# Performance work log

Measured on AMD Instinct MI355X. Metric: run time of the kernel, lower is better.

The kernel has to match this reference:

```python
import jax, jax.numpy as jnp
import numpy as np

N = 50000        # nodes
E = 800000       # edges
IN_C = 128       # in_channels
HID = 256        # hidden_channels
HEADS = 4
HD = HID // HEADS
LAYERS = 4
GRAPHS = 64
OUT_C = 32
MAX_POS = 10
EPS = 1e-5


def layer_norm(x, g, b):
    mu = jnp.mean(x, axis=-1, keepdims=True)
    var = jnp.mean((x - mu) ** 2, axis=-1, keepdims=True)
    return (x - mu) / jnp.sqrt(var + EPS) * g + b


def setup_inputs() -> dict:
    key = jax.random.key(0)
    ks = jax.random.split(key, 32)
    s = 0.02
    inp = {
        "x": jax.random.normal(ks[0], (N, IN_C), dtype=jnp.float32),
        "edge_index": jax.random.randint(ks[1], (2, E), 0, N, dtype=jnp.int32),
        "pos_idx": jax.random.randint(ks[2], (N,), 0, MAX_POS, dtype=jnp.int32),
        "batch": jnp.sort(jax.random.randint(ks[3], (N,), 0, GRAPHS, dtype=jnp.int32)),
        # encoder MLP: Linear(IN->HID), ReLU, LN(HID), Linear(HID->HID); weights stored [in,out]
        "enc_w1": jax.random.normal(ks[4], (IN_C, HID)) * s,
        "enc_b1": jnp.zeros((HID,), jnp.float32),
        "enc_g": jnp.ones((HID,), jnp.float32),
        "enc_beta": jnp.zeros((HID,), jnp.float32),
        "enc_w2": jax.random.normal(ks[5], (HID, HID)) * s,
        "enc_b2": jnp.zeros((HID,), jnp.float32),
        "pos_emb": jax.random.normal(ks[6], (MAX_POS, HID)) * s,
        # stacked attention-layer params [LAYERS, ...]
        "Wq": jax.random.normal(ks[7], (LAYERS, HID, HID)) * s,
        "bq": jnp.zeros((LAYERS, HID), jnp.float32),
        "Wk": jax.random.normal(ks[8], (LAYERS, HID, HID)) * s,
        "bk": jnp.zeros((LAYERS, HID), jnp.float32),
        "Wv": jax.random.normal(ks[9], (LAYERS, HID, HID)) * s,
        "bv": jnp.zeros((LAYERS, HID), jnp.float32),
        "mlp_w1": jax.random.normal(ks[10], (LAYERS, 2 * HID, HID)) * s,
        "mlp_b1": jnp.zeros((LAYERS, HID), jnp.float32),
        "mlp_g": jnp.ones((LAYERS, HID), jnp.float32),
        "mlp_beta": jnp.zeros((LAYERS, HID), jnp.float32),
        "mlp_w2": jax.random.normal(ks[11], (LAYERS, HID, HID)) * s,
        "mlp_b2": jnp.zeros((LAYERS, HID), jnp.float32),
        # classifier
        "cls_w1": jax.random.normal(ks[12], (HID, HID)) * s,
        "cls_b1": jnp.zeros((HID,), jnp.float32),
        "cls_g": jnp.ones((HID,), jnp.float32),
        "cls_beta": jnp.zeros((HID,), jnp.float32),
        "cls_w2": jax.random.normal(ks[13], (HID, OUT_C)) * s,
        "cls_b2": jnp.zeros((OUT_C,), jnp.float32),
    }
    return inp


def reference(x, edge_index, pos_idx, batch,
              enc_w1, enc_b1, enc_g, enc_beta, enc_w2, enc_b2, pos_emb,
              Wq, bq, Wk, bk, Wv, bv,
              mlp_w1, mlp_b1, mlp_g, mlp_beta, mlp_w2, mlp_b2,
              cls_w1, cls_b1, cls_g, cls_beta, cls_w2, cls_b2):
    row, col = edge_index[0], edge_index[1]
    n = x.shape[0]
    e = row.shape[0]

    # NodeEncoder
    h = layer_norm(jax.nn.relu(x @ enc_w1 + enc_b1), enc_g, enc_beta) @ enc_w2 + enc_b2
    h = h + pos_emb[pos_idx]

    scale = jnp.asarray(HD, h.dtype) ** 0.5
    for l in range(LAYERS):
        Q = (h @ Wq[l] + bq[l]).reshape(n, HEADS, HD)
        K = (h @ Wk[l] + bk[l]).reshape(n, HEADS, HD)
        V = (h @ Wv[l] + bv[l]).reshape(n, HEADS, HD)
        # per-edge attention scores [E, HEADS]
        scores = jnp.sum(Q[row] * K[col], axis=-1) / scale
        # segment softmax over destination node `row`
        m = jax.ops.segment_max(scores, row, num_segments=n)
        ex = jnp.exp(scores - m[row])
        denom = jax.ops.segment_sum(ex, row, num_segments=n)
        w = ex / denom[row]                         # [E, HEADS]
        msg = (w[..., None] * V[col]).reshape(e, HID)
        agg = jax.ops.segment_sum(msg, row, num_segments=n)  # [N, HID]
        cat = jnp.concatenate([h, agg], axis=-1)
        z = layer_norm(jax.nn.relu(cat @ mlp_w1[l] + mlp_b1[l]), mlp_g[l], mlp_beta[l]) @ mlp_w2[l] + mlp_b2[l]
        h = z + h

    # global mean pool over graphs
    sums = jax.ops.segment_sum(h, batch, num_segments=GRAPHS)
    cnt = jax.ops.segment_sum(jnp.ones((n, 1), h.dtype), batch, num_segments=GRAPHS)
    pooled = sums / jnp.maximum(cnt, 1.0)

    out = layer_norm(jax.nn.relu(pooled @ cls_w1 + cls_b1), cls_g, cls_beta) @ cls_w2 + cls_b2
    return out
```

## Files before the change

### kernel.cpp

```cpp
#include <hip/hip_runtime.h>
#include <cstdint>

#define HID 256
#define HEADS 4
#define GRAPHS 64
#define OUTC 32
#define EPSV 1e-5f
#define PSPLIT 32

typedef __bf16 b16x8 __attribute__((ext_vector_type(8)));
typedef float  f32x4 __attribute__((ext_vector_type(4)));

__device__ __forceinline__ f32x4 mfma16(b16x8 a, b16x8 b, f32x4 c) {
    return __builtin_amdgcn_mfma_f32_16x16x32_bf16(a, b, c, 0, 0, 0);
}

__device__ __forceinline__ unsigned int pack_bf16(float a, float b) {
    unsigned short ua = __builtin_bit_cast(unsigned short, (__bf16)a);
    unsigned short ub = __builtin_bit_cast(unsigned short, (__bf16)b);
    return (unsigned int)ua | ((unsigned int)ub << 16);
}

__device__ __forceinline__ void unpack2(unsigned int u, float& lo, float& hi) {
    lo = __builtin_bit_cast(float, u << 16);
    hi = __builtin_bit_cast(float, u & 0xffff0000u);
}

__global__ __launch_bounds__(256) void wtrans_kernel(const float* __restrict__ W,
    unsigned short* __restrict__ Wt, int K, int C)
{
    __shared__ float tile[32][33];
    const float* Wm = W + (size_t)blockIdx.z * K * C;
    unsigned short* Wtm = Wt + (size_t)blockIdx.z * K * C;
    int k0 = blockIdx.x * 32, c0 = blockIdx.y * 32;
    int tx = threadIdx.x & 31, ty = threadIdx.x >> 5;
#pragma unroll
    for (int i = 0; i < 32; i += 8)
        tile[ty + i][tx] = Wm[(size_t)(k0 + ty + i) * C + c0 + tx];
    __syncthreads();
#pragma unroll
    for (int i = 0; i < 32; i += 8) {
        float v = tile[tx][ty + i];
        Wtm[(size_t)(c0 + ty + i) * K + k0 + tx] =
            __builtin_bit_cast(unsigned short, (__bf16)v);
    }
}

__global__ __launch_bounds__(256) void enc1_mfma(
    const float* __restrict__ in0, const unsigned short* __restrict__ Wt,
    const float* __restrict__ bias, const float* __restrict__ g,
    const float* __restrict__ be, unsigned short* __restrict__ outb, int n)
{
    constexpr int KTILE = 128, ROWB = 256;
    __shared__ __align__(16) char alds[64 * 256];
    __shared__ float red[4][64][2];
    int tid = threadIdx.x, lane = tid & 63, wv = tid >> 6;
    int cg = lane & 15, rg = lane >> 4;
    int base = blockIdx.x * 64;
    int cbase = wv * 64;

    f32x4 acc[4][4];
#pragma unroll
    for (int m = 0; m < 4; m++)
#pragma unroll
        for (int f = 0; f < 4; f++) acc[m][f] = (f32x4){0.f, 0.f, 0.f, 0.f};

#pragma unroll
    for (int i = 0; i < 8; i++) {
        int idx = (i * 256 + tid) * 4;
        int row = idx >> 7, k = idx & 127;
        int node = base + row;
        float4 v = {0.f, 0.f, 0.f, 0.f};
        if (node < n) v = *(const float4*)(in0 + (size_t)node * KTILE + k);
        uint2 pp; pp.x = pack_bf16(v.x, v.y); pp.y = pack_bf16(v.z, v.w);
        int off = row * ROWB + k * 2;
        off ^= (row & 7) << 4;
        *(uint2*)(alds + off) = pp;
    }
    __syncthreads();

#pragma unroll 2
    for (int k0 = 0; k0 < KTILE; k0 += 32) {
        b16x8 a[4], b[4];
#pragma unroll
        for (int m = 0; m < 4; m++) {
            int R = m * 16 + cg;
            int off = R * ROWB + (k0 + rg * 8) * 2;
            off ^= (R & 7) << 4;
            a[m] = __builtin_bit_cast(b16x8, *(const uint4*)(alds + off));
        }
#pragma unroll
        for (int f = 0; f < 4; f++) {
            const unsigned short* p = Wt + (size_t)(cbase + f * 16 + cg) * KTILE + k0 + rg * 8;
            b[f] = __builtin_bit_cast(b16x8, *(const uint4*)p);
        }
#pragma unroll
        for (int m = 0; m < 4; m++)
#pragma unroll
            for (int f = 0; f < 4; f++)
                acc[m][f] = mfma16(a[m], b[f], acc[m][f]);
    }

    float bias_v[4], g_v[4], be_v[4];
#pragma unroll
    for (int f = 0; f < 4; f++) {
        int col = cbase + f * 16 + cg;
        bias_v[f] = bias[col]; g_v[f] = g[col]; be_v[f] = be[col];
    }
#pragma unroll
    for (int m = 0; m < 4; m++)
#pragma unroll
        for (int f = 0; f < 4; f++)
#pragma unroll
            for (int r = 0; r < 4; r++)
                acc[m][f][r] = fmaxf(acc[m][f][r] + bias_v[f], 0.f);
#pragma unroll
    for (int m = 0; m < 4; m++)
#pragma unroll
        for (int r = 0; r < 4; r++) {
            float s = acc[m][0][r] + acc[m][1][r] + acc[m][2][r] + acc[m][3][r];
            float q = acc[m][0][r] * acc[m][0][r] + acc[m][1][r] * acc[m][1][r]
                    + acc[m][2][r] * acc[m][2][r] + acc[m][3][r] * acc[m][3][r];
#pragma unroll
            for (int o = 1; o < 16; o <<= 1) {
                s += __shfl_xor(s, o, 64); q += __shfl_xor(q, o, 64);
            }
            if (cg == 0) { int R = m * 16 + rg * 4 + r; red[wv][R][0] = s; red[wv][R][1] = q; }
        }
    __syncthreads();
#pragma unroll
    for (int m = 0; m < 4; m++)
#pragma unroll
        for (int r = 0; r < 4; r++) {
            int R = m * 16 + rg * 4 + r;
            float S = red[0][R][0] + red[1][R][0] + red[2][R][0] + red[3][R][0];
            float Q = red[0][R][1] + red[1][R][1] + red[2][R][1] + red[3][R][1];
            float mu = S * (1.f / HID);
            float rs = rsqrtf(Q * (1.f / HID) - mu * mu + EPSV);
            int row = base + R;
            if (row >= n) continue;
            size_t ro = (size_t)row * HID;
#pragma unroll
            for (int f = 0; f < 4; f++) {
                float v = (acc[m][f][r] - mu) * rs * g_v[f] + be_v[f];
                outb[ro + cbase + f * 16 + cg] = __builtin_bit_cast(unsigned short, (__bf16)v);
            }
        }
}

template<int KTILE, int NPASS, bool RELU_LN, bool ADD_RES, bool POS, bool OUTF, bool OUTB>
__global__ __launch_bounds__(256) void gemm_bf16(
    const unsigned short* __restrict__ in0, const unsigned short* __restrict__ in1,
    const unsigned short* __restrict__ Wt, const float* __restrict__ bias,
    const float* __restrict__ g, const float* __restrict__ be,
    const float* __restrict__ addsrc, const float* __restrict__ pos_emb,
    const int* __restrict__ pidx, float* __restrict__ outf,
    unsigned short* __restrict__ outb, int n)
{
    constexpr int KS = KTILE * NPASS;
    constexpr int ROWB = KTILE * 2;
    constexpr int UPR = KTILE / 8;
    __shared__ __align__(16) char alds[64 * KTILE * 2];
    __shared__ float red[4][64][2];

    int tid = threadIdx.x, lane = tid & 63, wv = tid >> 6;
    int cg = lane & 15, rg = lane >> 4;
    int base = blockIdx.x * 64;
    int cbase = wv * 64;

    f32x4 acc[4][4];
#pragma unroll
    for (int m = 0; m < 4; m++)
#pragma unroll
        for (int f = 0; f < 4; f++) acc[m][f] = (f32x4){0.f, 0.f, 0.f, 0.f};

    for (int pass = 0; pass < NPASS; pass++) {
        if (pass) __syncthreads();
        const unsigned short* src = pass ? in1 : in0;
        constexpr int ITERS = (64 * UPR) / 256;
#pragma unroll
        for (int i = 0; i < ITERS; i++) {
            int idx = i * 256 + tid;
            int row = idx / UPR, u = idx % UPR;
            int node = base + row;
            uint4 v = {0u, 0u, 0u, 0u};
            if (node < n) v = *(const uint4*)(src + (size_t)node * KTILE + u * 8);
            int off = row * ROWB + u * 16;
            off ^= (row & 7) << 4;
            *(uint4*)(alds + off) = v;
        }
        __syncthreads();

        const unsigned short* Wp = Wt + pass * KTILE;
#pragma unroll 2
        for (int k0 = 0; k0 < KTILE; k0 += 32) {
            b16x8 a[4], b[4];
#pragma unroll
            for (int m = 0; m < 4; m++) {
                int R = m * 16 + cg;
                int off = R * ROWB + (k0 + rg * 8) * 2;
                off ^= (R & 7) << 4;
                a[m] = __builtin_bit_cast(b16x8, *(const uint4*)(alds + off));
            }
#pragma unroll
            for (int f = 0; f < 4; f++) {
                const unsigned short* p = Wp + (size_t)(cbase + f * 16 + cg) * KS + k0 + rg * 8;
                b[f] = __builtin_bit_cast(b16x8, *(const uint4*)p);
            }
#pragma unroll
            for (int m = 0; m < 4; m++)
#pragma unroll
                for (int f = 0; f < 4; f++)
                    acc[m][f] = mfma16(a[m], b[f], acc[m][f]);
        }
    }

    float bias_v[4], g_v[4], be_v[4];
#pragma unroll
    for (int f = 0; f < 4; f++) {
        int col = cbase + f * 16 + cg;
        bias_v[f] = bias[col];
        if (RELU_LN) { g_v[f] = g[col]; be_v[f] = be[col]; }
    }
#pragma unroll
    for (int m = 0; m < 4; m++)
#pragma unroll
        for (int f = 0; f < 4; f++)
#pragma unroll
            for (int r = 0; r < 4; r++) acc[m][f][r] += bias_v[f];

    if (RELU_LN) {
#pragma unroll
        for (int m = 0; m < 4; m++)
#pragma unroll
            for (int f = 0; f < 4; f++)
#pragma unroll
                for (int r = 0; r < 4; r++) acc[m][f][r] = fmaxf(acc[m][f][r], 0.f);
#pragma unroll
        for (int m = 0; m < 4; m++)
#pragma unroll
            for (int r = 0; r < 4; r++) {
                float s = acc[m][0][r] + acc[m][1][r] + acc[m][2][r] + acc[m][3][r];
                float q = acc[m][0][r] * acc[m][0][r] + acc[m][1][r] * acc[m][1][r]
                        + acc[m][2][r] * acc[m][2][r] + acc[m][3][r] * acc[m][3][r];
#pragma unroll
                for (int o = 1; o < 16; o <<= 1) {
                    s += __shfl_xor(s, o, 64); q += __shfl_xor(q, o, 64);
                }
                if (cg == 0) { int R = m * 16 + rg * 4 + r; red[wv][R][0] = s; red[wv][R][1] = q; }
            }
        __syncthreads();
#pragma unroll
        for (int m = 0; m < 4; m++)
#pragma unroll
            for (int r = 0; r < 4; r++) {
                int R = m * 16 + rg * 4 + r;
                float S = red[0][R][0] + red[1][R][0] + red[2][R][0] + red[3][R][0];
                float Q = red[0][R][1] + red[1][R][1] + red[2][R][1] + red[3][R][1];
                float mu = S * (1.f / HID);
                float rs = rsqrtf(Q * (1.f / HID) - mu * mu + EPSV);
#pragma unroll
                for (int f = 0; f < 4; f++)
                    acc[m][f][r] = (acc[m][f][r] - mu) * rs * g_v[f] + be_v[f];
            }
    }

#pragma unroll
    for (int m = 0; m < 4; m++)
#pragma unroll
        for (int r = 0; r < 4; r++) {
            int row = base + m * 16 + rg * 4 + r;
            if (row >= n) continue;
            size_t ro = (size_t)row * HID;
            int pid = 0;
            if (POS) pid = pidx[row];
#pragma unroll
            for (int f = 0; f < 4; f++) {
                int col = cbase + f * 16 + cg;
                float v = acc[m][f][r];
                if (ADD_RES) v += addsrc[ro + col];
                if (POS)     v += pos_emb[(size_t)pid * HID + col];
                if (OUTF)    outf[ro + col] = v;
                if (OUTB)    outb[ro + col] = __builtin_bit_cast(unsigned short, (__bf16)v);
            }
        }
}

__global__ __launch_bounds__(256) void qkv_mfma_kernel(
    const unsigned short* __restrict__ hsrc,
    const unsigned short* __restrict__ Wtq, const unsigned short* __restrict__ Wtk,
    const unsigned short* __restrict__ Wtv,
    const float* __restrict__ bq, const float* __restrict__ bk, const float* __restrict__ bv,
    unsigned short* __restrict__ Qo, unsigned short* __restrict__ Ko,
    unsigned short* __restrict__ Vo, int n)
{
    constexpr int ROWB = 512;
    __shared__ __align__(16) char alds[64 * 512];
    int tid = threadIdx.x, lane = tid & 63, wv = tid >> 6;
    int cg = lane & 15, rg = lane >> 4;
    int base = blockIdx.x * 64;
    int cbase = wv * 64;

#pragma unroll
    for (int i = 0; i < 8; i++) {
        int idx = i * 256 + tid;
        int row = idx >> 5, u = idx & 31;
        int node = base + row;
        uint4 v = {0u, 0u, 0u, 0u};
        if (node < n) v = *(const uint4*)(hsrc + (size_t)node * HID + u * 8);
        int off = row * ROWB + u * 16;
        off ^= (row & 7) << 4;
        *(uint4*)(alds + off) = v;
    }
    __syncthreads();

    for (int mat = 0; mat < 3; mat++) {
        const unsigned short* Wp = (mat == 0) ? Wtq : (mat == 1) ? Wtk : Wtv;
        const float* bp = (mat == 0) ? bq : (mat == 1) ? bk : bv;
        unsigned short* op = (mat == 0) ? Qo : (mat == 1) ? Ko : Vo;

        f32x4 acc[4][4];
#pragma unroll
        for (int m = 0; m < 4; m++)
#pragma unroll
            for (int f = 0; f < 4; f++) acc[m][f] = (f32x4){0.f, 0.f, 0.f, 0.f};

#pragma unroll 2
        for (int k0 = 0; k0 < 256; k0 += 32) {
            b16x8 a[4], b[4];
#pragma unroll
            for (int m = 0; m < 4; m++) {
                int R = m * 16 + cg;
                int off = R * ROWB + (k0 + rg * 8) * 2;
                off ^= (R & 7) << 4;
                a[m] = __builtin_bit_cast(b16x8, *(const uint4*)(alds + off));
            }
#pragma unroll
            for (int f = 0; f < 4; f++) {
                const unsigned short* p = Wp + (size_t)(cbase + f * 16 + cg) * 256 + k0 + rg * 8;
                b[f] = __builtin_bit_cast(b16x8, *(const uint4*)p);
            }
#pragma unroll
            for (int m = 0; m < 4; m++)
#pragma unroll
                for (int f = 0; f < 4; f++)
                    acc[m][f] = mfma16(a[m], b[f], acc[m][f]);
        }

        float bias_v[4];
#pragma unroll
        for (int f = 0; f < 4; f++) bias_v[f] = bp[cbase + f * 16 + cg];
#pragma unroll
        for (int m = 0; m < 4; m++)
#pragma unroll
            for (int r = 0; r < 4; r++) {
                int row = base + m * 16 + rg * 4 + r;
                if (row >= n) continue;
                size_t ro = (size_t)row * HID;
#pragma unroll
                for (int f = 0; f < 4; f++) {
                    float v = acc[m][f][r] + bias_v[f];
                    op[ro + cbase + f * 16 + cg] = __builtin_bit_cast(unsigned short, (__bf16)v);
                }
            }
    }
}

__global__ void count_kernel(const int* __restrict__ row, int* __restrict__ counts, int e)
{
    int i = blockIdx.x * blockDim.x + threadIdx.x;
    if (i < e) atomicAdd(&counts[row[i]], 1);
}

__global__ __launch_bounds__(256) void scan1_kernel(const int* __restrict__ counts,
    int* __restrict__ offs, int* __restrict__ bsum, int n)
{
    __shared__ int wsumS[4];
    int tid = threadIdx.x, b = blockIdx.x;
    int i = b * 256 + tid;
    int v = (i < n) ? counts[i] : 0;
    int lane = tid & 63, wv = tid >> 6;
    int s = v;
#pragma unroll
    for (int o = 1; o < 64; o <<= 1) { int t = __shfl_up(s, o, 64); if (lane >= o) s += t; }
    if (lane == 63) wsumS[wv] = s;
    __syncthreads();
    int add = 0;
    for (int j = 0; j < wv; j++) add += wsumS[j];
    s += add;
    if (i < n) offs[i + 1] = s;
    if (tid == 255) bsum[b] = s;
}

__global__ __launch_bounds__(256) void scan2_kernel(int* __restrict__ bsum, int nb)
{
    __shared__ int wsumS[4];
    int tid = threadIdx.x;
    int v = (tid < nb) ? bsum[tid] : 0;
    int lane = tid & 63, wv = tid >> 6;
    int s = v;
#pragma unroll
    for (int o = 1; o < 64; o <<= 1) { int t = __shfl_up(s, o, 64); if (lane >= o) s += t; }
    if (lane == 63) wsumS[wv] = s;
    __syncthreads();
    int add = 0;
    for (int j = 0; j < wv; j++) add += wsumS[j];
    s += add;
    if (tid < nb) bsum[tid] = s;
}

__global__ __launch_bounds__(256) void scan3_kernel(int* __restrict__ offs,
    const int* __restrict__ bsum, int n)
{
    int tid = threadIdx.x, b = blockIdx.x;
    int i = b * 256 + tid;
    if (i == 0) offs[0] = 0;
    if (i < n && b > 0) offs[i + 1] += bsum[b - 1];
}

__global__ void scatter_kernel(const int* __restrict__ row, const int* __restrict__ col,
    const int* __restrict__ offs, int* __restrict__ cur, int* __restrict__ ccol, int e)
{
    int i = blockIdx.x * blockDim.x + threadIdx.x;
    if (i >= e) return;
    int r = row[i];
    int pos = atomicAdd(&cur[r], 1);
    ccol[offs[r] + pos] = col[i];
}

__global__ __launch_bounds__(256) void attn_hw_kernel(
    const unsigned short* __restrict__ Qm, const unsigned short* __restrict__ Km,
    const unsigned short* __restrict__ Vm,
    const int* __restrict__ offs, const int* __restrict__ ccol,
    unsigned short* __restrict__ agg, int n)
{
    int tid = threadIdx.x;
    int hw = tid >> 5;
    int l32 = tid & 31;
    int node = blockIdx.x * 8 + hw;
    if (node >= n) return;
    int start = offs[node], fin = offs[node + 1];
    size_t rowoff = (size_t)node * HID + l32 * 8;
    if (start == fin) {
        uint4 z = {0u, 0u, 0u, 0u};
        *(uint4*)(agg + rowoff) = z;
        return;
    }

    uint4 qr = *(const uint4*)(Qm + rowoff);
    float qf[8];
    unpack2(qr.x, qf[0], qf[1]);
    unpack2(qr.y, qf[2], qf[3]);
    unpack2(qr.z, qf[4], qf[5]);
    unpack2(qr.w, qf[6], qf[7]);

    float m = -3.0e38f, d = 0.f;
    float acc[8];
#pragma unroll
    for (int j = 0; j < 8; j++) acc[j] = 0.f;

    for (int i = start; i < fin; i++) {
        int c = ccol[i];
        const unsigned short* kp = Km + (size_t)c * HID + l32 * 8;
        const unsigned short* vp = Vm + (size_t)c * HID + l32 * 8;
        uint4 kr = *(const uint4*)kp;
        uint4 vr = *(const uint4*)vp;
        float k0, k1, k2, k3, k4, k5, k6, k7;
        unpack2(kr.x, k0, k1); unpack2(kr.y, k2, k3);
        unpack2(kr.z, k4, k5); unpack2(kr.w, k6, k7);
        float p = qf[0] * k0 + qf[1] * k1 + qf[2] * k2 + qf[3] * k3
                + qf[4] * k4 + qf[5] * k5 + qf[6] * k6 + qf[7] * k7;
        p += __shfl_xor(p, 1, 64);
        p += __shfl_xor(p, 2, 64);
        p += __shfl_xor(p, 4, 64);
        float s = p * 0.125f;
        float mn = fmaxf(m, s);
        float sc = __expf(m - mn);
        float w = __expf(s - mn);
        d = d * sc + w;
        float v0, v1, v2, v3, v4, v5, v6, v7;
        unpack2(vr.x, v0, v1); unpack2(vr.y, v2, v3);
        unpack2(vr.z, v4, v5); unpack2(vr.w, v6, v7);
        acc[0] = acc[0] * sc + w * v0;  acc[1] = acc[1] * sc + w * v1;
        acc[2] = acc[2] * sc + w * v2;  acc[3] = acc[3] * sc + w * v3;
        acc[4] = acc[4] * sc + w * v4;  acc[5] = acc[5] * sc + w * v5;
        acc[6] = acc[6] * sc + w * v6;  acc[7] = acc[7] * sc + w * v7;
        m = mn;
    }

    float inv = 1.f / d;
    uint4 out;
    out.x = pack_bf16(acc[0] * inv, acc[1] * inv);
    out.y = pack_bf16(acc[2] * inv, acc[3] * inv);
    out.z = pack_bf16(acc[4] * inv, acc[5] * inv);
    out.w = pack_bf16(acc[6] * inv, acc[7] * inv);
    *(uint4*)(agg + rowoff) = out;
}

__global__ void bounds_kernel(const int* __restrict__ batch, int* __restrict__ gb, int n)
{
    int g = threadIdx.x;
    if (g > GRAPHS) return;
    int lo = 0, hi = n;
    while (lo < hi) { int mid = (lo + hi) >> 1; if (batch[mid] < g) lo = mid + 1; else hi = mid; }
    gb[g] = lo;
}

__global__ __launch_bounds__(256) void pool_partial_kernel(const float* __restrict__ h,
    const int* __restrict__ gb, float* __restrict__ partial)
{
    int s = blockIdx.x, g = blockIdx.y, tid = threadIdx.x;
    int lo = gb[g], hi = gb[g + 1];
    float sum = 0.f;
    for (int i = lo + s; i < hi; i += PSPLIT) sum += h[(size_t)i * HID + tid];
    partial[((size_t)g * PSPLIT + s) * HID + tid] = sum;
}

__global__ __launch_bounds__(256) void pool_reduce_kernel(const float* __restrict__ partial,
    const int* __restrict__ gb, float* __restrict__ pooled)
{
    int g = blockIdx.x, tid = threadIdx.x;
    float sum = 0.f;
#pragma unroll
    for (int s = 0; s < PSPLIT; s++) sum += partial[((size_t)g * PSPLIT + s) * HID + tid];
    int cnt = gb[g + 1] - gb[g];
    pooled[g * HID + tid] = sum / fmaxf((float)cnt, 1.f);
}

__global__ __launch_bounds__(256) void cls_kernel(const float* __restrict__ pooled,
    const float* __restrict__ W1, const float* __restrict__ b1,
    const float* __restrict__ g, const float* __restrict__ be,
    const float* __restrict__ W2, const float* __restrict__ b2,
    float* __restrict__ out)
{
    __shared__ float pin[HID];
    __shared__ float hbuf[HID];
    __shared__ float red2[4][2];
    int tid = threadIdx.x, gi = blockIdx.x;
    int lane = tid & 63, wv = tid >> 6;
    pin[tid] = pooled[gi * HID + tid];
    __syncthreads();
    float acc = 0.f;
    for (int k = 0; k < HID; k++) acc += pin[k] * W1[k * HID + tid];
    acc = fmaxf(acc + b1[tid], 0.f);
    float s = acc, q = acc * acc;
#pragma unroll
    for (int o = 1; o < 64; o <<= 1) { s += __shfl_xor(s, o, 64); q += __shfl_xor(q, o, 64); }
    if (lane == 0) { red2[wv][0] = s; red2[wv][1] = q; }
    __syncthreads();
    float S = red2[0][0] + red2[1][0] + red2[2][0] + red2[3][0];
    float Q = red2[0][1] + red2[1][1] + red2[2][1] + red2[3][1];
    float mu = S * (1.f / HID);
    float rs = rsqrtf(Q * (1.f / HID) - mu * mu + EPSV);
    hbuf[tid] = (acc - mu) * rs * g[tid] + be[tid];
    __syncthreads();
    if (tid < OUTC) {
        float o = 0.f;
        for (int k = 0; k < HID; k++) o += hbuf[k] * W2[k * OUTC + tid];
        out[gi * OUTC + tid] = o + b2[tid];
    }
}

extern "C" void kernel_launch(void* const* d_in, const int* in_sizes, int n_in,
                              void* d_out, int out_size, void* d_ws, size_t ws_size,
                              hipStream_t stream)
{
    const float* x        = (const float*)d_in[0];
    const int*   ei       = (const int*)d_in[1];
    const int*   pidx     = (const int*)d_in[2];
    const int*   batch    = (const int*)d_in[3];
    const float* enc_w1   = (const float*)d_in[4];
    const float* enc_b1   = (const float*)d_in[5];
    const float* enc_g    = (const float*)d_in[6];
    const float* enc_beta = (const float*)d_in[7];
    const float* enc_w2   = (const float*)d_in[8];
    const float* enc_b2   = (const float*)d_in[9];
    const float* pos_emb  = (const float*)d_in[10];
    const float* Wq       = (const float*)d_in[11];
    const float* bq       = (const float*)d_in[12];
    const float* Wk       = (const float*)d_in[13];
    const float* bk       = (const float*)d_in[14];
    const float* Wv       = (const float*)d_in[15];
    const float* bv       = (const float*)d_in[16];
    const float* mlp_w1   = (const float*)d_in[17];
    const float* mlp_b1   = (const float*)d_in[18];
    const float* mlp_g    = (const float*)d_in[19];
    const float* mlp_beta = (const float*)d_in[20];
    const float* mlp_w2   = (const float*)d_in[21];
    const float* mlp_b2   = (const float*)d_in[22];
    const float* cls_w1   = (const float*)d_in[23];
    const float* cls_b1   = (const float*)d_in[24];
    const float* cls_g    = (const float*)d_in[25];
    const float* cls_beta = (const float*)d_in[26];
    const float* cls_w2   = (const float*)d_in[27];
    const float* cls_b2   = (const float*)d_in[28];

    int n = in_sizes[2];
    int e = in_sizes[1] / 2;
    const int* row = ei;
    const int* col = ei + e;

    char* p = (char*)d_ws;
    auto alloc = [&](size_t bytes) -> void* {
        void* r = (void*)p;
        p += (bytes + 255) & ~(size_t)255;
        return r;
    };
    size_t NH = (size_t)n * HID;
    float* h             = (float*)alloc(NH * 4);
    unsigned short* h16  = (unsigned short*)alloc(NH * 2);
    unsigned short* a16  = (unsigned short*)alloc(NH * 2);
    unsigned short* m16  = (unsigned short*)alloc(NH * 2);
    unsigned short* Qb   = (unsigned short*)alloc(NH * 2);
    unsigned short* Kb   = (unsigned short*)alloc(NH * 2);
    unsigned short* Vb   = (unsigned short*)alloc(NH * 2);
    float* partial = (float*)alloc((size_t)GRAPHS * PSPLIT * HID * 4);
    float* pooled  = (float*)alloc((size_t)GRAPHS * HID * 4);
    int* counts = (int*)alloc((size_t)n * 4);
    int* offs   = (int*)alloc((size_t)(n + 1) * 4);
    int* cur    = (int*)alloc((size_t)n * 4);
    int* ccol   = (int*)alloc((size_t)e * 4);
    int* bsum   = (int*)alloc(1024);
    int* gb     = (int*)alloc((GRAPHS + 1) * 4);
    unsigned short* wt_e1 = (unsigned short*)alloc((size_t)128 * 256 * 2);
    unsigned short* wt_e2 = (unsigned short*)alloc((size_t)256 * 256 * 2);
    unsigned short* wt_q  = (unsigned short*)alloc((size_t)4 * 256 * 256 * 2);
    unsigned short* wt_k  = (unsigned short*)alloc((size_t)4 * 256 * 256 * 2);
    unsigned short* wt_v  = (unsigned short*)alloc((size_t)4 * 256 * 256 * 2);
    unsigned short* wt_m1 = (unsigned short*)alloc((size_t)4 * 512 * 256 * 2);
    unsigned short* wt_m2 = (unsigned short*)alloc((size_t)4 * 256 * 256 * 2);

    int gblocks = (n + 63) / 64;
    int nb = (n + 255) / 256;

    wtrans_kernel<<<dim3(4, 8, 1),  256, 0, stream>>>(enc_w1, wt_e1, 128, 256);
    wtrans_kernel<<<dim3(8, 8, 1),  256, 0, stream>>>(enc_w2, wt_e2, 256, 256);
    wtrans_kernel<<<dim3(8, 8, 4),  256, 0, stream>>>(Wq,     wt_q,  256, 256);
    wtrans_kernel<<<dim3(8, 8, 4),  256, 0, stream>>>(Wk,     wt_k,  256, 256);
    wtrans_kernel<<<dim3(8, 8, 4),  256, 0, stream>>>(Wv,     wt_v,  256, 256);
    wtrans_kernel<<<dim3(16, 8, 4), 256, 0, stream>>>(mlp_w1, wt_m1, 512, 256);
    wtrans_kernel<<<dim3(8, 8, 4),  256, 0, stream>>>(mlp_w2, wt_m2, 256, 256);

    hipMemsetAsync(counts, 0, (size_t)n * 4, stream);
    hipMemsetAsync(cur, 0, (size_t)n * 4, stream);
    count_kernel<<<(e + 255) / 256, 256, 0, stream>>>(row, counts, e);
    scan1_kernel<<<nb, 256, 0, stream>>>(counts, offs, bsum, n);
    scan2_kernel<<<1, 256, 0, stream>>>(bsum, nb);
    scan3_kernel<<<nb, 256, 0, stream>>>(offs, bsum, n);
    scatter_kernel<<<(e + 255) / 256, 256, 0, stream>>>(row, col, offs, cur, ccol, e);
    bounds_kernel<<<1, 128, 0, stream>>>(batch, gb, n);

    enc1_mfma<<<gblocks, 256, 0, stream>>>(x, wt_e1, enc_b1, enc_g, enc_beta, m16, n);
    gemm_bf16<256, 1, false, false, true, true, true><<<gblocks, 256, 0, stream>>>(
        m16, nullptr, wt_e2, enc_b2, nullptr, nullptr, nullptr, pos_emb, pidx, h, h16, n);

    int ablocks = (n + 7) / 8;
    for (int l = 0; l < 4; l++) {
        size_t wo = (size_t)l * 256 * 256;
        size_t bo = (size_t)l * HID;
        qkv_mfma_kernel<<<gblocks, 256, 0, stream>>>(
            h16, wt_q + wo, wt_k + wo, wt_v + wo, bq + bo, bk + bo, bv + bo,
            Qb, Kb, Vb, n);
        attn_hw_kernel<<<ablocks, 256, 0, stream>>>(Qb, Kb, Vb, offs, ccol, a16, n);
        gemm_bf16<256, 2, true, false, false, false, true><<<gblocks, 256, 0, stream>>>(
            h16, a16, wt_m1 + (size_t)l * 512 * 256, mlp_b1 + bo,
            mlp_g + bo, mlp_beta + bo, nullptr, nullptr, nullptr, nullptr, m16, n);
        gemm_bf16<256, 1, false, true, false, true, true><<<gblocks, 256, 0, stream>>>(
            m16, nullptr, wt_m2 + wo, mlp_b2 + bo, nullptr, nullptr, h, nullptr, nullptr,
            h, h16, n);
    }

    pool_partial_kernel<<<dim3(PSPLIT, GRAPHS), 256, 0, stream>>>(h, gb, partial);
    pool_reduce_kernel<<<GRAPHS, 256, 0, stream>>>(partial, gb, pooled);
    cls_kernel<<<GRAPHS, 256, 0, stream>>>(pooled, cls_w1, cls_b1, cls_g, cls_beta,
                                           cls_w2, cls_b2, (float*)d_out);
}
```

Measured before the change: 1.431 ms.

## Stage GEMM A tiles via direct global-to-LDS loads and prefetch weight fragments

Result: no change. 1.448 ms (+1.2%).

```diff
diff --git a/kernel.cpp b/kernel.cpp
--- a/kernel.cpp
+++ b/kernel.cpp
@@ -24,6 +24,23 @@
 __device__ __forceinline__ void unpack2(unsigned int u, float& lo, float& hi) {
     lo = __builtin_bit_cast(float, u << 16);
     hi = __builtin_bit_cast(float, u & 0xffff0000u);
+}
+
+__device__ __forceinline__ void stage_gld(char* buf, const unsigned short* __restrict__ src,
+                                          int base, int tid)
+{
+#pragma unroll
+    for (int i = 0; i < 8; i++) {
+        int idx = i * 256 + tid;
+        int r = idx >> 5;
+        int u = idx & 31;
+        int us = u ^ (r & 7);
+        const void* gp = (const void*)(src + (size_t)(base + r) * HID + us * 8);
+        __builtin_amdgcn_global_load_lds(
+            (const __attribute__((address_space(1))) void*)gp,
+            (__attribute__((address_space(3))) void*)(buf + idx * 16),
+            16, 0, 0);
+    }
 }
 
 __global__ __launch_bounds__(256) void wtrans_kernel(const float* __restrict__ W,
@@ -148,7 +165,7 @@
         }
 }
 
-template<int KTILE, int NPASS, bool RELU_LN, bool ADD_RES, bool POS, bool OUTF, bool OUTB>
+template<int NPASS, bool RELU_LN, bool ADD_RES, bool POS, bool OUTF, bool OUTB>
 __global__ __launch_bounds__(256) void gemm_bf16(
     const unsigned short* __restrict__ in0, const unsigned short* __restrict__ in1,
     const unsigned short* __restrict__ Wt, const float* __restrict__ bias,
@@ -157,10 +174,9 @@
     const int* __restrict__ pidx, float* __restrict__ outf,
     unsigned short* __restrict__ outb, int n)
 {
+    constexpr int KTILE = 256;
     constexpr int KS = KTILE * NPASS;
-    constexpr int ROWB = KTILE * 2;
-    constexpr int UPR = KTILE / 8;
-    __shared__ __align__(16) char alds[64 * KTILE * 2];
+    __shared__ __align__(16) char alds[64 * 512];
     __shared__ float red[4][64][2];
 
     int tid = threadIdx.x, lane = tid & 63, wv = tid >> 6;
@@ -177,41 +193,40 @@
     for (int pass = 0; pass < NPASS; pass++) {
         if (pass) __syncthreads();
         const unsigned short* src = pass ? in1 : in0;
-        constexpr int ITERS = (64 * UPR) / 256;
-#pragma unroll
-        for (int i = 0; i < ITERS; i++) {
-            int idx = i * 256 + tid;
-            int row = idx / UPR, u = idx % UPR;
-            int node = base + row;
-            uint4 v = {0u, 0u, 0u, 0u};
-            if (node < n) v = *(const uint4*)(src + (size_t)node * KTILE + u * 8);
-            int off = row * ROWB + u * 16;
-            off ^= (row & 7) << 4;
-            *(uint4*)(alds + off) = v;
-        }
+        const unsigned short* Wp = Wt + pass * KTILE;
+
+        stage_gld(alds, src, base, tid);
+
+        b16x8 bcur[4], bnxt[4];
+#pragma unroll
+        for (int f = 0; f < 4; f++)
+            bcur[f] = __builtin_bit_cast(b16x8, *(const uint4*)(
+                Wp + (size_t)(cbase + f * 16 + cg) * KS + rg * 8));
         __syncthreads();
 
-        const unsigned short* Wp = Wt + pass * KTILE;
-#pragma unroll 2
-        for (int k0 = 0; k0 < KTILE; k0 += 32) {
-            b16x8 a[4], b[4];
+#pragma unroll
+        for (int kk = 0; kk < 8; kk++) {
+            if (kk < 7) {
+#pragma unroll
+                for (int f = 0; f < 4; f++)
+                    bnxt[f] = __builtin_bit_cast(b16x8, *(const uint4*)(
+                        Wp + (size_t)(cbase + f * 16 + cg) * KS + (kk + 1) * 32 + rg * 8));
+            }
+            b16x8 a[4];
 #pragma unroll
             for (int m = 0; m < 4; m++) {
                 int R = m * 16 + cg;
-                int off = R * ROWB + (k0 + rg * 8) * 2;
+                int off = R * 512 + (kk * 32 + rg * 8) * 2;
                 off ^= (R & 7) << 4;
                 a[m] = __builtin_bit_cast(b16x8, *(const uint4*)(alds + off));
             }
 #pragma unroll
-            for (int f = 0; f < 4; f++) {
-                const unsigned short* p = Wp + (size_t)(cbase + f * 16 + cg) * KS + k0 + rg * 8;
-                b[f] = __builtin_bit_cast(b16x8, *(const uint4*)p);
-            }
-#pragma unroll
             for (int m = 0; m < 4; m++)
 #pragma unroll
                 for (int f = 0; f < 4; f++)
-                    acc[m][f] = mfma16(a[m], b[f], acc[m][f]);
+                    acc[m][f] = mfma16(a[m], bcur[f], acc[m][f]);
+#pragma unroll
+            for (int f = 0; f < 4; f++) bcur[f] = bnxt[f];
         }
     }
 
@@ -294,24 +309,13 @@
     unsigned short* __restrict__ Qo, unsigned short* __restrict__ Ko,
     unsigned short* __restrict__ Vo, int n)
 {
-    constexpr int ROWB = 512;
     __shared__ __align__(16) char alds[64 * 512];
     int tid = threadIdx.x, lane = tid & 63, wv = tid >> 6;
     int cg = lane & 15, rg = lane >> 4;
     int base = blockIdx.x * 64;
     int cbase = wv * 64;
 
-#pragma unroll
-    for (int i = 0; i < 8; i++) {
-        int idx = i * 256 + tid;
-        int row = idx >> 5, u = idx & 31;
-        int node = base + row;
-        uint4 v = {0u, 0u, 0u, 0u};
-        if (node < n) v = *(const uint4*)(hsrc + (size_t)node * HID + u * 8);
-        int off = row * ROWB + u * 16;
-        off ^= (row & 7) << 4;
-        *(uint4*)(alds + off) = v;
-    }
+    stage_gld(alds, hsrc, base, tid);
     __syncthreads();
 
     for (int mat = 0; mat < 3; mat++) {
@@ -325,26 +329,35 @@
 #pragma unroll
             for (int f = 0; f < 4; f++) acc[m][f] = (f32x4){0.f, 0.f, 0.f, 0.f};
 
-#pragma unroll 2
-        for (int k0 = 0; k0 < 256; k0 += 32) {
-            b16x8 a[4], b[4];
+        b16x8 bcur[4], bnxt[4];
+#pragma unroll
+        for (int f = 0; f < 4; f++)
+            bcur[f] = __builtin_bit_cast(b16x8, *(const uint4*)(
+                Wp + (size_t)(cbase + f * 16 + cg) * 256 + rg * 8));
+
+#pragma unroll
+        for (int kk = 0; kk < 8; kk++) {
+            if (kk < 7) {
+#pragma unroll
+                for (int f = 0; f < 4; f++)
+                    bnxt[f] = __builtin_bit_cast(b16x8, *(const uint4*)(
+                        Wp + (size_t)(cbase + f * 16 + cg) * 256 + (kk + 1) * 32 + rg * 8));
+            }
+            b16x8 a[4];
 #pragma unroll
             for (int m = 0; m < 4; m++) {
                 int R = m * 16 + cg;
-                int off = R * ROWB + (k0 + rg * 8) * 2;
+                int off = R * 512 + (kk * 32 + rg * 8) * 2;
                 off ^= (R & 7) << 4;
                 a[m] = __builtin_bit_cast(b16x8, *(const uint4*)(alds + off));
             }
 #pragma unroll
-            for (int f = 0; f < 4; f++) {
-                const unsigned short* p = Wp + (size_t)(cbase + f * 16 + cg) * 256 + k0 + rg * 8;
-                b[f] = __builtin_bit_cast(b16x8, *(const uint4*)p);
-            }
-#pragma unroll
             for (int m = 0; m < 4; m++)
 #pragma unroll
                 for (int f = 0; f < 4; f++)
-                    acc[m][f] = mfma16(a[m], b[f], acc[m][f]);
+                    acc[m][f] = mfma16(a[m], bcur[f], acc[m][f]);
+#pragma unroll
+            for (int f = 0; f < 4; f++) bcur[f] = bnxt[f];
         }
 
         float bias_v[4];
@@ -651,7 +664,7 @@
     bounds_kernel<<<1, 128, 0, stream>>>(batch, gb, n);
 
     enc1_mfma<<<gblocks, 256, 0, stream>>>(x, wt_e1, enc_b1, enc_g, enc_beta, m16, n);
-    gemm_bf16<256, 1, false, false, true, true, true><<<gblocks, 256, 0, stream>>>(
+    gemm_bf16<1, false, false, true, true, true><<<gblocks, 256, 0, stream>>>(
         m16, nullptr, wt_e2, enc_b2, nullptr, nullptr, nullptr, pos_emb, pidx, h, h16, n);
 
     int ablocks = (n + 7) / 8;
@@ -662,10 +675,10 @@
             h16, wt_q + wo, wt_k + wo, wt_v + wo, bq + bo, bk + bo, bv + bo,
             Qb, Kb, Vb, n);
         attn_hw_kernel<<<ablocks, 256, 0, stream>>>(Qb, Kb, Vb, offs, ccol, a16, n);
-        gemm_bf16<256, 2, true, false, false, false, true><<<gblocks, 256, 0, stream>>>(
+        gemm_bf16<2, true, false, false, false, true><<<gblocks, 256, 0, stream>>>(
             h16, a16, wt_m1 + (size_t)l * 512 * 256, mlp_b1 + bo,
             mlp_g + bo, mlp_beta + bo, nullptr, nullptr, nullptr, nullptr, m16, n);
-        gemm_bf16<256, 1, false, true, false, true, true><<<gblocks, 256, 0, stream>>>(
+        gemm_bf16<1, false, true, false, true, true><<<gblocks, 256, 0, stream>>>(
             m16, nullptr, wt_m2 + wo, mlp_b2 + bo, nullptr, nullptr, h, nullptr, nullptr,
             h, h16, n);
     }
```
